# Performance work log

Measured on AMD Instinct MI355X. Metric: run time of the kernel, lower is better.

The kernel has to match this reference:

```python
import jax, jax.numpy as jnp
import numpy as np

B, S, D_IN, D_OUT, H = 4, 2048, 1024, 1024, 16
HD = D_OUT // H  # head_dim = 64


def setup_inputs() -> dict:
    key = jax.random.key(0)
    ks = jax.random.split(key, 6)
    scale = 1.0 / np.sqrt(D_IN)
    return {
        "x": jax.random.normal(ks[0], (B, S, D_IN), dtype=jnp.float32),
        "Wq": jax.random.normal(ks[1], (D_IN, D_OUT), dtype=jnp.float32) * scale,
        "Wk": jax.random.normal(ks[2], (D_IN, D_OUT), dtype=jnp.float32) * scale,
        "Wv": jax.random.normal(ks[3], (D_IN, D_OUT), dtype=jnp.float32) * scale,
        "Wo": jax.random.normal(ks[4], (D_OUT, D_OUT), dtype=jnp.float32) * (1.0 / np.sqrt(D_OUT)),
        "bo": jax.random.normal(ks[5], (D_OUT,), dtype=jnp.float32) * 0.02,
    }


def reference(x, Wq, Wk, Wv, Wo, bo):
    b, n, _ = x.shape
    h, hd = H, HD
    # projections -> (b, h, n, hd)
    q = (x @ Wq).reshape(b, n, h, hd).transpose(0, 2, 1, 3)
    k = (x @ Wk).reshape(b, n, h, hd).transpose(0, 2, 1, 3)
    v = (x @ Wv).reshape(b, n, h, hd).transpose(0, 2, 1, 3)
    # scores (b, h, n, n) with causal mask then scale (matches original order)
    scores = jnp.einsum("bhqd,bhkd->bhqk", q, k)
    causal = jnp.tril(jnp.ones((n, n), dtype=bool))  # True = keep
    scores = jnp.where(causal, scores, -jnp.inf) / jnp.sqrt(jnp.asarray(hd, x.dtype))
    attn = jax.nn.softmax(scores, axis=-1)
    ctx = jnp.einsum("bhqk,bhkd->bhqd", attn, v)
    ctx = ctx.transpose(0, 2, 1, 3).reshape(b, n, h * hd)
    return ctx @ Wo + bo
```

## Files before the change

kernel.cpp:

```cpp
#include <hip/hip_runtime.h>
#include <hip/hip_bf16.h>
#include <math.h>

typedef __attribute__((ext_vector_type(4))) float f32x4;
typedef __attribute__((ext_vector_type(16))) float f32x16;
typedef __attribute__((ext_vector_type(8))) short bf16x8;
typedef __attribute__((ext_vector_type(4))) unsigned int u32x4;

#define DEV __device__ __forceinline__
#define MFMA16 __builtin_amdgcn_mfma_f32_16x16x32_bf16
#define MFMA32 __builtin_amdgcn_mfma_f32_32x32x16_bf16
#define SBAR __builtin_amdgcn_s_barrier()
#define SCHED0 __builtin_amdgcn_sched_barrier(0)
#define LGKM0 asm volatile("s_waitcnt lgkmcnt(0)" ::: "memory")

constexpr int S      = 2048;
constexpr int DMODEL = 1024;
constexpr int HD     = 64;
constexpr int MROWS  = 4 * 2048;

DEV unsigned short f2bf(float f) {
  union { float f; unsigned int u; } v; v.f = f;
  unsigned int u = v.u;
  unsigned int r = u + 0x7fffu + ((u >> 16) & 1u);
  return (unsigned short)(r >> 16);
}

DEV unsigned int pkbf(float lo, float hi) {
  unsigned int r;
  asm("v_cvt_pk_bf16_f32 %0, %1, %2" : "=v"(r) : "v"(lo), "v"(hi));
  return r;
}

DEV float fexp2(float x) { return __builtin_amdgcn_exp2f(x); }

DEV void gload_lds16(const void* g, void* l) {
  __builtin_amdgcn_global_load_lds(
      (const __attribute__((address_space(1))) unsigned int*)g,
      (__attribute__((address_space(3))) unsigned int*)l, 16, 0, 0);
}

__global__ __launch_bounds__(256) void k_conv(const float* __restrict__ in,
                                              unsigned short* __restrict__ out) {
  int i = blockIdx.x * 256 + threadIdx.x;
  float4 v = ((const float4*)in)[i];
  ushort4 o;
  o.x = f2bf(v.x); o.y = f2bf(v.y); o.z = f2bf(v.z); o.w = f2bf(v.w);
  ((ushort4*)out)[i] = o;
}

__global__ __launch_bounds__(256) void k_transpose4(const float* __restrict__ Wq,
                                                    const float* __restrict__ Wk,
                                                    const float* __restrict__ Wv,
                                                    const float* __restrict__ Wo,
                                                    unsigned short* __restrict__ wt,
                                                    unsigned short* __restrict__ wot) {
  __shared__ float tile[32][33];
  const int z = blockIdx.z;
  const float* W = (z == 0) ? Wq : (z == 1) ? Wk : (z == 2) ? Wv : Wo;
  unsigned short* Wt = (z == 3) ? wot : wt + (size_t)z * DMODEL * DMODEL;
  int n0 = blockIdx.x * 32, k0 = blockIdx.y * 32;
  int tx = threadIdx.x, ty = threadIdx.y;
#pragma unroll
  for (int j = 0; j < 4; ++j)
    tile[ty + j * 8][tx] = W[(size_t)(k0 + ty + j * 8) * DMODEL + n0 + tx];
  __syncthreads();
#pragma unroll
  for (int j = 0; j < 4; ++j)
    Wt[(size_t)(n0 + ty + j * 8) * DMODEL + k0 + tx] = f2bf(tile[tx][ty + j * 8]);
}

__global__ __launch_bounds__(512, 1) void k_gemmQ8(const unsigned short* __restrict__ A,
                                                   const unsigned short* __restrict__ Bt,
                                                   unsigned short* __restrict__ Qg,
                                                   unsigned short* __restrict__ Kg,
                                                   unsigned short* __restrict__ Vt) {
  __shared__ __align__(16) char lds[163840];
  const int tid = threadIdx.x, lane = tid & 63;
  const int wid = tid >> 6, wm = wid >> 2, wn = wid & 3;
  const int lq = lane & 15, lg = lane >> 4;
  constexpr int NBX = 8;
  const int flat = blockIdx.x;
  const int wg = (flat & 7) * 32 + (flat >> 3);
  const int by = wg / NBX, bx = wg % NBX;
  const int m0 = by * 256, n0 = bx * 384;

  auto stageA = [&](int kt, int unit) {
    char* dA = lds + (kt & 1) * 81920;
    const unsigned short* gA = A + (size_t)m0 * DMODEL + kt * 64;
    int c = tid + unit * 512; int r = c >> 3, cc = c & 7;
    gload_lds16(gA + (size_t)r * DMODEL + ((cc ^ (r & 7)) << 3), dA + c * 16);
  };
  auto stageB = [&](int kt, int unit) {
    char* dB = lds + (kt & 1) * 81920 + 32768;
    const unsigned short* gB = Bt + (size_t)n0 * DMODEL + kt * 64;
    int c = tid + unit * 512; int r = c >> 3, cc = c & 7;
    gload_lds16(gB + (size_t)r * DMODEL + ((cc ^ (r & 7)) << 3), dB + c * 16);
  };

#pragma unroll
  for (int u = 0; u < 4; ++u) stageA(0, u);
#pragma unroll
  for (int u = 0; u < 6; ++u) stageB(0, u);
#pragma unroll
  for (int u = 0; u < 4; ++u) stageA(1, u);
#pragma unroll
  for (int u = 0; u < 6; ++u) stageB(1, u);
  SCHED0;
  asm volatile("s_waitcnt vmcnt(10)" ::: "memory");
  SCHED0;
  SBAR;
  SCHED0;

  f32x4 acc[8][6] = {};
#pragma unroll 1
  for (int t = 0; t < 16; ++t) {
    const char* pA = lds + (t & 1) * 81920;
    const char* pB = pA + 32768;
    const bool sN = (t >= 1 && t < 15);
    bf16x8 bfr[6];
    {
      bf16x8 af[4];
#pragma unroll
      for (int mi = 0; mi < 4; ++mi) {
        int row = wm * 128 + mi * 16 + lq;
        af[mi] = *(const bf16x8*)(pA + row * 128 + ((lg ^ (row & 7)) << 4));
      }
#pragma unroll
      for (int ni = 0; ni < 6; ++ni) {
        int row = wn * 96 + ni * 16 + lq;
        bfr[ni] = *(const bf16x8*)(pB + row * 128 + ((lg ^ (row & 7)) << 4));
      }
      if (sN) { stageB(t + 1, 2); stageB(t + 1, 3); stageB(t + 1, 4); }
      SBAR; LGKM0; SCHED0;
      __builtin_amdgcn_s_setprio(1);
#pragma unroll
      for (int mi = 0; mi < 4; ++mi)
#pragma unroll
        for (int ni = 0; ni < 6; ++ni)
          acc[mi][ni] = MFMA16(af[mi], bfr[ni], acc[mi][ni], 0, 0, 0);
      __builtin_amdgcn_s_setprio(0);
      SCHED0;
    }
    {
      bf16x8 af[4];
#pragma unroll
      for (int mi = 0; mi < 4; ++mi) {
        int row = wm * 128 + (mi + 4) * 16 + lq;
        af[mi] = *(const bf16x8*)(pA + row * 128 + ((lg ^ (row & 7)) << 4));
      }
      if (sN) { stageB(t + 1, 5); stageA(t + 1, 0); stageA(t + 1, 1); }
      SBAR; LGKM0; SCHED0;
      __builtin_amdgcn_s_setprio(1);
#pragma unroll
      for (int mi = 0; mi < 4; ++mi)
#pragma unroll
        for (int ni = 0; ni < 6; ++ni)
          acc[mi + 4][ni] = MFMA16(af[mi], bfr[ni], acc[mi + 4][ni], 0, 0, 0);
      __builtin_amdgcn_s_setprio(0);
      SCHED0;
    }
    {
      bf16x8 af[4];
#pragma unroll
      for (int mi = 0; mi < 4; ++mi) {
        int row = wm * 128 + mi * 16 + lq;
        af[mi] = *(const bf16x8*)(pA + row * 128 + (((4 + lg) ^ (row & 7)) << 4));
      }
#pragma unroll
      for (int ni = 0; ni < 6; ++ni) {
        int row = wn * 96 + ni * 16 + lq;
        bfr[ni] = *(const bf16x8*)(pB + row * 128 + (((4 + lg) ^ (row & 7)) << 4));
      }
      if (sN) { stageA(t + 1, 2); stageA(t + 1, 3); }
      SBAR; LGKM0; SCHED0;
      __builtin_amdgcn_s_setprio(1);
#pragma unroll
      for (int mi = 0; mi < 4; ++mi)
#pragma unroll
        for (int ni = 0; ni < 6; ++ni)
          acc[mi][ni] = MFMA16(af[mi], bfr[ni], acc[mi][ni], 0, 0, 0);
      __builtin_amdgcn_s_setprio(0);
      SCHED0;
    }
    {
      bf16x8 af[4];
#pragma unroll
      for (int mi = 0; mi < 4; ++mi) {
        int row = wm * 128 + (mi + 4) * 16 + lq;
        af[mi] = *(const bf16x8*)(pA + row * 128 + (((4 + lg) ^ (row & 7)) << 4));
      }
      if (t < 14) { stageB(t + 2, 0); stageB(t + 2, 1); }
      SBAR; LGKM0; SCHED0;
      __builtin_amdgcn_s_setprio(1);
#pragma unroll
      for (int mi = 0; mi < 4; ++mi)
#pragma unroll
        for (int ni = 0; ni < 6; ++ni)
          acc[mi + 4][ni] = MFMA16(af[mi], bfr[ni], acc[mi + 4][ni], 0, 0, 0);
      __builtin_amdgcn_s_setprio(0);
      SCHED0;
    }
    if (t < 14) {
      asm volatile("s_waitcnt vmcnt(2)" ::: "memory");
    } else if (t == 14) {
      asm volatile("s_waitcnt vmcnt(0)" ::: "memory");
    }
    SCHED0;
    if (t < 15) SBAR;
    SCHED0;
  }

#pragma unroll
  for (int mi = 0; mi < 8; ++mi)
#pragma unroll
    for (int ni = 0; ni < 6; ++ni) {
      int n = n0 + wn * 96 + ni * 16 + lq;
      int widx = n >> 10, nn = n & 1023;
      int h = nn >> 6, d = nn & 63;
      int mbase = m0 + wm * 128 + mi * 16 + lg * 4;
      int b_ = mbase >> 11, s_ = mbase & 2047;
      if (widx == 2) {
        ushort4 o;
        o.x = f2bf(acc[mi][ni][0]);
        o.y = f2bf(acc[mi][ni][1]);
        o.z = f2bf(acc[mi][ni][2]);
        o.w = f2bf(acc[mi][ni][3]);
        *(ushort4*)(Vt + ((size_t)((b_ * 16 + h) * 64 + d)) * S + s_) = o;
      } else {
        unsigned short* dst = (widx == 0) ? Qg : Kg;
        float scale = (widx == 0) ? 0.18033688f : 1.0f;
#pragma unroll
        for (int r = 0; r < 4; ++r)
          dst[(size_t)((b_ * 16 + h) * 2048 + s_ + r) * HD + d] = f2bf(acc[mi][ni][r] * scale);
      }
    }
}

__global__ __launch_bounds__(512, 2) void k_gemmP(const unsigned short* __restrict__ A,
                                                  const unsigned short* __restrict__ Bt,
                                                  const float* __restrict__ bo,
                                                  float* __restrict__ out) {
  __shared__ __align__(16) char lds[147456];
  const int tid = threadIdx.x, lane = tid & 63;
  const int wid = tid >> 6, wm = wid >> 1, wn = wid & 1;
  const int lq = lane & 15, lg = lane >> 4;
  constexpr int NBX = 8;
  const int flat = blockIdx.x;
  const int wg = (flat & 7) * (NBX * 4) + (flat >> 3);
  const int by = wg / NBX, bx = wg % NBX;
  const int m0 = by * 256, n0 = bx * 128;

  auto stage = [&](int kt, int buf) {
    char* dA = lds + buf * 49152;
    char* dB = dA + 32768;
    const unsigned short* gA = A + (size_t)m0 * DMODEL + kt * 64;
    const unsigned short* gB = Bt + (size_t)n0 * DMODEL + kt * 64;
#pragma unroll
    for (int i = 0; i < 4; ++i) {
      int c = tid + i * 512; int r = c >> 3, cc = c & 7;
      gload_lds16(gA + (size_t)r * DMODEL + ((cc ^ (r & 7)) << 3), dA + c * 16);
    }
#pragma unroll
    for (int i = 0; i < 2; ++i) {
      int c = tid + i * 512; int r = c >> 3, cc = c & 7;
      gload_lds16(gB + (size_t)r * DMODEL + ((cc ^ (r & 7)) << 3), dB + c * 16);
    }
  };

  stage(0, 0);
  stage(1, 1);
  SCHED0;
  asm volatile("s_waitcnt vmcnt(6)" ::: "memory");
  SCHED0;
  SBAR;
  SCHED0;

  f32x4 acc[4][4] = {};
  int bcur = 0, bth = 2;
#pragma unroll 1
  for (int t = 0; t < 16; ++t) {
    if (t < 14) stage(t + 2, bth);
    const char* pA = lds + bcur * 49152;
    const char* pB = pA + 32768;
#pragma unroll
    for (int kk = 0; kk < 2; ++kk) {
      bf16x8 af[4], bfr[4];
#pragma unroll
      for (int mi = 0; mi < 4; ++mi) {
        int row = wm * 64 + mi * 16 + lq;
        af[mi] = *(const bf16x8*)(pA + row * 128 + ((((kk << 2) + lg) ^ (row & 7)) << 4));
      }
#pragma unroll
      for (int ni = 0; ni < 4; ++ni) {
        int row = wn * 64 + ni * 16 + lq;
        bfr[ni] = *(const bf16x8*)(pB + row * 128 + ((((kk << 2) + lg) ^ (row & 7)) << 4));
      }
      __builtin_amdgcn_s_setprio(1);
#pragma unroll
      for (int mi = 0; mi < 4; ++mi)
#pragma unroll
        for (int ni = 0; ni < 4; ++ni)
          acc[mi][ni] = MFMA16(af[mi], bfr[ni], acc[mi][ni], 0, 0, 0);
      __builtin_amdgcn_s_setprio(0);
    }
    SCHED0;
    if (t < 14) {
      asm volatile("s_waitcnt vmcnt(6)" ::: "memory");
    } else if (t == 14) {
      asm volatile("s_waitcnt vmcnt(0)" ::: "memory");
    }
    SCHED0;
    if (t < 15) SBAR;
    SCHED0;
    int nb = (bcur + 1 == 3) ? 0 : bcur + 1;
    int nt = (bth + 1 == 3) ? 0 : bth + 1;
    bcur = nb; bth = nt;
  }

#pragma unroll
  for (int mi = 0; mi < 4; ++mi)
#pragma unroll
    for (int ni = 0; ni < 4; ++ni) {
      int n = n0 + wn * 64 + ni * 16 + lq;
      float bv = bo[n];
#pragma unroll
      for (int r = 0; r < 4; ++r) {
        int m = m0 + wm * 64 + mi * 16 + lg * 4 + r;
        out[(size_t)m * DMODEL + n] = acc[mi][ni][r] + bv;
      }
    }
}

__global__ __launch_bounds__(512, 2) void k_attn(const unsigned short* __restrict__ Qg,
                                                 const unsigned short* __restrict__ Kg,
                                                 const unsigned short* __restrict__ Vt,
                                                 unsigned short* __restrict__ Ctx) {
  __shared__ __align__(16) char lds[32768];
  const int f = blockIdx.x;
  const int i4 = f & 255, hi2 = f >> 8;
  const int bh = i4 >> 2, q = i4 & 3;
  const int Qb = hi2 ? (7 - q) : q;
  const int tid = threadIdx.x;
  const int lane = tid & 63, w = tid >> 6;
  const int lq5 = lane & 31, hi = lane >> 5;
  const size_t base = (size_t)bh * (S * HD);
  const int b = bh >> 4, h = bh & 15;
  const int krow = tid >> 3, kcc = tid & 7, scc = kcc ^ (krow & 7);
  const int vd = tid >> 3;
  const int vfd = (vd & 7) ^ ((vd >> 3) & 7);
  const int vscc = (tid & 7) ^ vfd;
  const unsigned short* VtRow = Vt + (size_t)(bh * 64 + vd) * S;

  const int q0w = Qb * 256 + w * 32;
  const int tmax = 4 * Qb + 3;
  const int diag = q0w >> 6;

  bf16x8 qF[4];
#pragma unroll
  for (int dc = 0; dc < 4; ++dc)
    qF[dc] = *(const bf16x8*)(Qg + base + (size_t)(q0w + lq5) * HD + dc * 16 + hi * 8);

  f32x16 o0 = {}, o1 = {};
  float m_run = -INFINITY, l_run = 0.f;

  gload_lds16(Kg + base + (size_t)krow * HD + scc * 8, lds + tid * 16);
  gload_lds16(VtRow + vscc * 8, lds + 16384 + tid * 16);
  __syncthreads();

#pragma unroll 1
  for (int t = 0; t <= tmax; ++t) {
    const int cur = t & 1, nxt = cur ^ 1;
    char* sK  = lds + cur * 8192;
    char* sVT = lds + 16384 + cur * 8192;
    const bool have_next = (t < tmax);
    if (have_next) {
      gload_lds16(Kg + base + (size_t)((t + 1) * 64 + krow) * HD + scc * 8,
                  lds + nxt * 8192 + tid * 16);
      gload_lds16(VtRow + (t + 1) * 64 + vscc * 8,
                  lds + 16384 + nxt * 8192 + tid * 16);
    }
    const bool active = (t <= diag);
    if (active) {
      const bool isdiag = (t == diag);
      const int nkb = (isdiag && !(q0w & 32)) ? 1 : 2;
      f32x16 st0 = {}, st1 = {};
#pragma unroll
      for (int dc = 0; dc < 4; ++dc) {
        int row = lq5;
        bf16x8 a0 = *(const bf16x8*)(sK + row * 128 + (((2 * dc + hi) ^ (row & 7)) << 4));
        st0 = MFMA32(a0, qF[dc], st0, 0, 0, 0);
      }
      if (nkb == 2) {
#pragma unroll
        for (int dc = 0; dc < 4; ++dc) {
          int row = 32 + lq5;
          bf16x8 a1 = *(const bf16x8*)(sK + row * 128 + (((2 * dc + hi) ^ (row & 7)) << 4));
          st1 = MFMA32(a1, qF[dc], st1, 0, 0, 0);
        }
      }
      if (isdiag) {
        int qo = q0w + lq5 - t * 64;
        if (q0w & 32) {
#pragma unroll
          for (int r = 0; r < 16; ++r) {
            int key = 32 + (r & 3) + 8 * (r >> 2) + 4 * hi;
            st1[r] = (key > qo) ? -INFINITY : st1[r];
          }
        } else {
#pragma unroll
          for (int r = 0; r < 16; ++r) {
            int key = (r & 3) + 8 * (r >> 2) + 4 * hi;
            st0[r] = (key > qo) ? -INFINITY : st0[r];
          }
        }
      }
      float mx = st0[0];
#pragma unroll
      for (int r = 1; r < 16; ++r) mx = fmaxf(mx, st0[r]);
      if (nkb == 2) {
#pragma unroll
        for (int r = 0; r < 16; ++r) mx = fmaxf(mx, st1[r]);
      }
      mx = fmaxf(mx, __shfl_xor(mx, 32));
      bool need = !(mx <= m_run + 8.0f);
      if (__any(need)) {
        float mn = fmaxf(m_run, mx);
        float alpha = fexp2(m_run - mn);
        m_run = mn;
        l_run *= alpha;
#pragma unroll
        for (int r = 0; r < 16; ++r) { o0[r] *= alpha; o1[r] *= alpha; }
      }
      float rs[4] = {0.f, 0.f, 0.f, 0.f};
#pragma unroll
      for (int r = 0; r < 16; ++r) {
        float p = fexp2(st0[r] - m_run);
        st0[r] = p;
        rs[r & 3] += p;
      }
      if (nkb == 2) {
#pragma unroll
        for (int r = 0; r < 16; ++r) {
          float p = fexp2(st1[r] - m_run);
          st1[r] = p;
          rs[r & 3] += p;
        }
      }
      float rsum = (rs[0] + rs[1]) + (rs[2] + rs[3]);
      rsum += __shfl_xor(rsum, 32);
      l_run += rsum;
      {
        unsigned int wv[8];
#pragma unroll
        for (int j = 0; j < 8; ++j) wv[j] = pkbf(st0[2 * j], st0[2 * j + 1]);
        asm("v_permlane32_swap_b32 %0, %1" : "+v"(wv[0]), "+v"(wv[2]));
        asm("v_permlane32_swap_b32 %0, %1" : "+v"(wv[1]), "+v"(wv[3]));
        asm("v_permlane32_swap_b32 %0, %1" : "+v"(wv[4]), "+v"(wv[6]));
        asm("v_permlane32_swap_b32 %0, %1" : "+v"(wv[5]), "+v"(wv[7]));
        union { bf16x8 v; unsigned int u[4]; } fa, fb;
        fa.u[0] = wv[0]; fa.u[1] = wv[1]; fa.u[2] = wv[2]; fa.u[3] = wv[3];
        fb.u[0] = wv[4]; fb.u[1] = wv[5]; fb.u[2] = wv[6]; fb.u[3] = wv[7];
#pragma unroll
        for (int kc = 0; kc < 2; ++kc) {
          bf16x8 bp = kc ? fb.v : fa.v;
          {
            int d = lq5, fd = (d & 7) ^ ((d >> 3) & 7);
            bf16x8 av = *(const bf16x8*)(sVT + d * 128 + (((kc * 2 + hi) ^ fd) << 4));
            o0 = MFMA32(av, bp, o0, 0, 0, 0);
          }
          {
            int d = 32 + lq5, fd = (d & 7) ^ ((d >> 3) & 7);
            bf16x8 av = *(const bf16x8*)(sVT + d * 128 + (((kc * 2 + hi) ^ fd) << 4));
            o1 = MFMA32(av, bp, o1, 0, 0, 0);
          }
        }
      }
      if (nkb == 2) {
        unsigned int wv[8];
#pragma unroll
        for (int j = 0; j < 8; ++j) wv[j] = pkbf(st1[2 * j], st1[2 * j + 1]);
        asm("v_permlane32_swap_b32 %0, %1" : "+v"(wv[0]), "+v"(wv[2]));
        asm("v_permlane32_swap_b32 %0, %1" : "+v"(wv[1]), "+v"(wv[3]));
        asm("v_permlane32_swap_b32 %0, %1" : "+v"(wv[4]), "+v"(wv[6]));
        asm("v_permlane32_swap_b32 %0, %1" : "+v"(wv[5]), "+v"(wv[7]));
        union { bf16x8 v; unsigned int u[4]; } fa, fb;
        fa.u[0] = wv[0]; fa.u[1] = wv[1]; fa.u[2] = wv[2]; fa.u[3] = wv[3];
        fb.u[0] = wv[4]; fb.u[1] = wv[5]; fb.u[2] = wv[6]; fb.u[3] = wv[7];
#pragma unroll
        for (int kc = 0; kc < 2; ++kc) {
          bf16x8 bp = kc ? fb.v : fa.v;
          {
            int d = lq5, fd = (d & 7) ^ ((d >> 3) & 7);
            bf16x8 av = *(const bf16x8*)(sVT + d * 128 + ((((2 + kc) * 2 + hi) ^ fd) << 4));
            o0 = MFMA32(av, bp, o0, 0, 0, 0);
          }
          {
            int d = 32 + lq5, fd = (d & 7) ^ ((d >> 3) & 7);
            bf16x8 av = *(const bf16x8*)(sVT + d * 128 + ((((2 + kc) * 2 + hi) ^ fd) << 4));
            o1 = MFMA32(av, bp, o1, 0, 0, 0);
          }
        }
      }
    }
    __syncthreads();
  }

  __syncthreads();
  {
    float inv = 1.0f / l_run;
    char* slice = lds + w * 4096;
#pragma unroll
    for (int db = 0; db < 2; ++db)
#pragma unroll
      for (int j = 0; j < 8; ++j) {
        int d0 = (j & 1) * 2 + (j >> 1) * 8 + 4 * hi + 32 * db;
        float va = (db ? o1[2 * j] : o0[2 * j]) * inv;
        float vb = (db ? o1[2 * j + 1] : o0[2 * j + 1]) * inv;
        *(unsigned int*)(slice + lq5 * 128 + (((d0 >> 3) ^ (lq5 & 7)) << 4) + (d0 & 7) * 2) =
            pkbf(va, vb);
      }
    asm volatile("s_waitcnt lgkmcnt(0)" ::: "memory");
#pragma unroll
    for (int i = 0; i < 4; ++i) {
      int r = lane >> 1, cc = (lane & 1) * 4 + i;
      u32x4 v = *(const u32x4*)(slice + r * 128 + ((cc ^ (r & 7)) << 4));
      *(u32x4*)(Ctx + (size_t)(b * S + q0w + r) * DMODEL + h * HD + cc * 8) = v;
    }
  }
}

extern "C" void kernel_launch(void* const* d_in, const int* in_sizes, int n_in,
                              void* d_out, int out_size, void* d_ws, size_t ws_size,
                              hipStream_t stream) {
  const float* x  = (const float*)d_in[0];
  const float* Wq = (const float*)d_in[1];
  const float* Wk = (const float*)d_in[2];
  const float* Wv = (const float*)d_in[3];
  const float* Wo = (const float*)d_in[4];
  const float* bo = (const float*)d_in[5];
  float* out = (float*)d_out;

  char* p = (char*)d_ws;
  unsigned short* xb  = (unsigned short*)p; p += (size_t)MROWS * DMODEL * 2;
  unsigned short* wt  = (unsigned short*)p; p += (size_t)3 * DMODEL * DMODEL * 2;
  unsigned short* wot = (unsigned short*)p; p += (size_t)DMODEL * DMODEL * 2;
  unsigned short* qg  = (unsigned short*)p; p += (size_t)MROWS * DMODEL * 2;
  unsigned short* kg  = (unsigned short*)p; p += (size_t)MROWS * DMODEL * 2;
  unsigned short* vt  = (unsigned short*)p; p += (size_t)MROWS * DMODEL * 2;
  unsigned short* ctx = (unsigned short*)p; p += (size_t)MROWS * DMODEL * 2;

  k_conv<<<(MROWS * DMODEL) / 1024, 256, 0, stream>>>(x, xb);
  k_transpose4<<<dim3(32, 32, 4), dim3(32, 8), 0, stream>>>(Wq, Wk, Wv, Wo, wt, wot);
  k_gemmQ8<<<256, 512, 0, stream>>>(xb, wt, qg, kg, vt);
  k_attn<<<512, 512, 0, stream>>>(qg, kg, vt, ctx);
  k_gemmP<<<256, 512, 0, stream>>>(ctx, wot, bo, out);
}
```

Baseline: 174.0 us.

## Halve QKV GEMM M-tile to 128 rows and launch 512 workgroups

The QKV projection GEMM tile shrinks from 256x384 to 128x384, so the grid doubles from 256 to 512 workgroups and more CUs get work (the device has 256 CUs). The k-step is restructured to reuse A fragments across two B halves, and the staging schedule and vmcnt waits are updated for the smaller A tile. This gives better occupancy and wave balance at the cost of lower arithmetic intensity and more redundant B loads per output.

```diff
diff --git a/kernel.cpp b/kernel.cpp
--- a/kernel.cpp
+++ b/kernel.cpp
@@ -75,129 +75,129 @@
                                                    unsigned short* __restrict__ Qg,
                                                    unsigned short* __restrict__ Kg,
                                                    unsigned short* __restrict__ Vt) {
-  __shared__ __align__(16) char lds[163840];
+  __shared__ __align__(16) char lds[131072];
   const int tid = threadIdx.x, lane = tid & 63;
   const int wid = tid >> 6, wm = wid >> 2, wn = wid & 3;
   const int lq = lane & 15, lg = lane >> 4;
   constexpr int NBX = 8;
   const int flat = blockIdx.x;
-  const int wg = (flat & 7) * 32 + (flat >> 3);
+  const int wg = (flat & 7) * 64 + (flat >> 3);
   const int by = wg / NBX, bx = wg % NBX;
-  const int m0 = by * 256, n0 = bx * 384;
+  const int m0 = by * 128, n0 = bx * 384;
 
   auto stageA = [&](int kt, int unit) {
-    char* dA = lds + (kt & 1) * 81920;
+    char* dA = lds + (kt & 1) * 65536;
     const unsigned short* gA = A + (size_t)m0 * DMODEL + kt * 64;
     int c = tid + unit * 512; int r = c >> 3, cc = c & 7;
     gload_lds16(gA + (size_t)r * DMODEL + ((cc ^ (r & 7)) << 3), dA + c * 16);
   };
   auto stageB = [&](int kt, int unit) {
-    char* dB = lds + (kt & 1) * 81920 + 32768;
+    char* dB = lds + (kt & 1) * 65536 + 16384;
     const unsigned short* gB = Bt + (size_t)n0 * DMODEL + kt * 64;
     int c = tid + unit * 512; int r = c >> 3, cc = c & 7;
     gload_lds16(gB + (size_t)r * DMODEL + ((cc ^ (r & 7)) << 3), dB + c * 16);
   };
 
 #pragma unroll
-  for (int u = 0; u < 4; ++u) stageA(0, u);
+  for (int u = 0; u < 2; ++u) stageA(0, u);
 #pragma unroll
   for (int u = 0; u < 6; ++u) stageB(0, u);
 #pragma unroll
-  for (int u = 0; u < 4; ++u) stageA(1, u);
+  for (int u = 0; u < 2; ++u) stageA(1, u);
 #pragma unroll
   for (int u = 0; u < 6; ++u) stageB(1, u);
   SCHED0;
-  asm volatile("s_waitcnt vmcnt(10)" ::: "memory");
+  asm volatile("s_waitcnt vmcnt(8)" ::: "memory");
   SCHED0;
   SBAR;
   SCHED0;
 
-  f32x4 acc[8][6] = {};
+  f32x4 acc[4][6] = {};
 #pragma unroll 1
   for (int t = 0; t < 16; ++t) {
-    const char* pA = lds + (t & 1) * 81920;
-    const char* pB = pA + 32768;
-    const bool sN = (t >= 1 && t < 15);
-    bf16x8 bfr[6];
+    const char* pA = lds + (t & 1) * 65536;
+    const char* pB = pA + 16384;
+    const bool sB = (t >= 1 && t <= 14);
+    bf16x8 af[4];
     {
-      bf16x8 af[4];
+      bf16x8 bfr[3];
 #pragma unroll
       for (int mi = 0; mi < 4; ++mi) {
-        int row = wm * 128 + mi * 16 + lq;
+        int row = wm * 64 + mi * 16 + lq;
         af[mi] = *(const bf16x8*)(pA + row * 128 + ((lg ^ (row & 7)) << 4));
       }
 #pragma unroll
-      for (int ni = 0; ni < 6; ++ni) {
+      for (int ni = 0; ni < 3; ++ni) {
         int row = wn * 96 + ni * 16 + lq;
         bfr[ni] = *(const bf16x8*)(pB + row * 128 + ((lg ^ (row & 7)) << 4));
       }
-      if (sN) { stageB(t + 1, 2); stageB(t + 1, 3); stageB(t + 1, 4); }
+      if (sB) { stageB(t + 1, 0); stageB(t + 1, 1); }
       SBAR; LGKM0; SCHED0;
       __builtin_amdgcn_s_setprio(1);
 #pragma unroll
       for (int mi = 0; mi < 4; ++mi)
 #pragma unroll
-        for (int ni = 0; ni < 6; ++ni)
+        for (int ni = 0; ni < 3; ++ni)
           acc[mi][ni] = MFMA16(af[mi], bfr[ni], acc[mi][ni], 0, 0, 0);
       __builtin_amdgcn_s_setprio(0);
       SCHED0;
     }
     {
-      bf16x8 af[4];
-#pragma unroll
-      for (int mi = 0; mi < 4; ++mi) {
-        int row = wm * 128 + (mi + 4) * 16 + lq;
-        af[mi] = *(const bf16x8*)(pA + row * 128 + ((lg ^ (row & 7)) << 4));
-      }
-      if (sN) { stageB(t + 1, 5); stageA(t + 1, 0); stageA(t + 1, 1); }
+      bf16x8 bfr[3];
+#pragma unroll
+      for (int ni = 0; ni < 3; ++ni) {
+        int row = wn * 96 + (ni + 3) * 16 + lq;
+        bfr[ni] = *(const bf16x8*)(pB + row * 128 + ((lg ^ (row & 7)) << 4));
+      }
+      if (sB) { stageB(t + 1, 2); stageB(t + 1, 3); }
       SBAR; LGKM0; SCHED0;
       __builtin_amdgcn_s_setprio(1);
 #pragma unroll
       for (int mi = 0; mi < 4; ++mi)
 #pragma unroll
-        for (int ni = 0; ni < 6; ++ni)
-          acc[mi + 4][ni] = MFMA16(af[mi], bfr[ni], acc[mi + 4][ni], 0, 0, 0);
+        for (int ni = 0; ni < 3; ++ni)
+          acc[mi][ni + 3] = MFMA16(af[mi], bfr[ni], acc[mi][ni + 3], 0, 0, 0);
       __builtin_amdgcn_s_setprio(0);
       SCHED0;
     }
     {
-      bf16x8 af[4];
+      bf16x8 bfr[3];
 #pragma unroll
       for (int mi = 0; mi < 4; ++mi) {
-        int row = wm * 128 + mi * 16 + lq;
+        int row = wm * 64 + mi * 16 + lq;
         af[mi] = *(const bf16x8*)(pA + row * 128 + (((4 + lg) ^ (row & 7)) << 4));
       }
 #pragma unroll
-      for (int ni = 0; ni < 6; ++ni) {
+      for (int ni = 0; ni < 3; ++ni) {
         int row = wn * 96 + ni * 16 + lq;
         bfr[ni] = *(const bf16x8*)(pB + row * 128 + (((4 + lg) ^ (row & 7)) << 4));
       }
-      if (sN) { stageA(t + 1, 2); stageA(t + 1, 3); }
+      if (sB) { stageB(t + 1, 4); stageB(t + 1, 5); }
       SBAR; LGKM0; SCHED0;
       __builtin_amdgcn_s_setprio(1);
 #pragma unroll
       for (int mi = 0; mi < 4; ++mi)
 #pragma unroll
-        for (int ni = 0; ni < 6; ++ni)
+        for (int ni = 0; ni < 3; ++ni)
           acc[mi][ni] = MFMA16(af[mi], bfr[ni], acc[mi][ni], 0, 0, 0);
       __builtin_amdgcn_s_setprio(0);
       SCHED0;
     }
     {
-      bf16x8 af[4];
-#pragma unroll
-      for (int mi = 0; mi < 4; ++mi) {
-        int row = wm * 128 + (mi + 4) * 16 + lq;
-        af[mi] = *(const bf16x8*)(pA + row * 128 + (((4 + lg) ^ (row & 7)) << 4));
-      }
-      if (t < 14) { stageB(t + 2, 0); stageB(t + 2, 1); }
+      bf16x8 bfr[3];
+#pragma unroll
+      for (int ni = 0; ni < 3; ++ni) {
+        int row = wn * 96 + (ni + 3) * 16 + lq;
+        bfr[ni] = *(const bf16x8*)(pB + row * 128 + (((4 + lg) ^ (row & 7)) << 4));
+      }
+      if (t < 14) { stageA(t + 2, 0); stageA(t + 2, 1); }
       SBAR; LGKM0; SCHED0;
       __builtin_amdgcn_s_setprio(1);
 #pragma unroll
       for (int mi = 0; mi < 4; ++mi)
 #pragma unroll
-        for (int ni = 0; ni < 6; ++ni)
-          acc[mi + 4][ni] = MFMA16(af[mi], bfr[ni], acc[mi + 4][ni], 0, 0, 0);
+        for (int ni = 0; ni < 3; ++ni)
+          acc[mi][ni + 3] = MFMA16(af[mi], bfr[ni], acc[mi][ni + 3], 0, 0, 0);
       __builtin_amdgcn_s_setprio(0);
       SCHED0;
     }
@@ -212,13 +212,13 @@
   }
 
 #pragma unroll
-  for (int mi = 0; mi < 8; ++mi)
+  for (int mi = 0; mi < 4; ++mi)
 #pragma unroll
     for (int ni = 0; ni < 6; ++ni) {
       int n = n0 + wn * 96 + ni * 16 + lq;
       int widx = n >> 10, nn = n & 1023;
       int h = nn >> 6, d = nn & 63;
-      int mbase = m0 + wm * 128 + mi * 16 + lg * 4;
+      int mbase = m0 + wm * 64 + mi * 16 + lg * 4;
       int b_ = mbase >> 11, s_ = mbase & 2047;
       if (widx == 2) {
         ushort4 o;
@@ -552,7 +552,7 @@
 
   k_conv<<<(MROWS * DMODEL) / 1024, 256, 0, stream>>>(x, xb);
   k_transpose4<<<dim3(32, 32, 4), dim3(32, 8), 0, stream>>>(Wq, Wk, Wv, Wo, wt, wot);
-  k_gemmQ8<<<256, 512, 0, stream>>>(xb, wt, qg, kg, vt);
+  k_gemmQ8<<<512, 512, 0, stream>>>(xb, wt, qg, kg, vt);
   k_attn<<<512, 512, 0, stream>>>(qg, kg, vt, ctx);
   k_gemmP<<<256, 512, 0, stream>>>(ctx, wot, bo, out);
 }
```

New measurement: 160.3 us. -7.9%, faster.
